# Kernel optimization log

Measured on AMD Instinct MI355X. Metric: run time of the kernel, lower is better.

## Reference

```python
import jax, jax.numpy as jnp
import numpy as np

N = 16384
H = 256
C = 2


def setup_inputs() -> dict:
    key = jax.random.key(0)
    ks = jax.random.split(key, 9)
    s = lambda fan_in: 1.0 / np.sqrt(fan_in)
    return {
        "coordinates": jax.random.normal(ks[0], (N, C), dtype=jnp.float32) * 10.0,
        "W1": jax.random.normal(ks[1], (C, H), dtype=jnp.float32) * s(C),
        "b1": jnp.zeros((H,), dtype=jnp.float32),
        "W2": jax.random.normal(ks[2], (H, H), dtype=jnp.float32) * s(H),
        "b2": jnp.zeros((H,), dtype=jnp.float32),
        "Wd1": jax.random.normal(ks[3], (1, H // 2), dtype=jnp.float32) * s(1),
        "bd1": jnp.zeros((H // 2,), dtype=jnp.float32),
        "Wd2": jax.random.normal(ks[4], (H // 2, H), dtype=jnp.float32) * s(H // 2),
        "bd2": jnp.zeros((H,), dtype=jnp.float32),
        "k": 6,
    }


def reference(coordinates, W1, b1, W2, b2, Wd1, bd1, Wd2, bd2, k):
    x = coordinates.astype(jnp.float32)
    # coord MLP: Linear -> SiLU -> Linear
    coord_emb = jax.nn.silu(x @ W1 + b1) @ W2 + b2  # (N, H)

    # pairwise Euclidean distances (N, N), via ||a||^2 + ||b||^2 - 2ab
    sq = jnp.sum(x * x, axis=1)  # (N,)
    d2 = sq[:, None] + sq[None, :] - 2.0 * (x @ x.T)
    dist = jnp.sqrt(jnp.maximum(d2, 1e-12))  # safe sqrt; diag ~ 0

    # k+1 smallest distances per row (includes self at ~0), ascending
    kk = min(k + 1, dist.shape[1])
    neg_top, _ = jax.lax.top_k(-dist, kk)
    topk_dist = -neg_top  # ascending smallest
    mean_dist = jnp.mean(topk_dist[:, 1:], axis=1, keepdims=True)  # (N, 1)

    dist_emb = jax.nn.silu(mean_dist @ Wd1 + bd1) @ Wd2 + bd2  # (N, H)
    return coord_emb + dist_emb
```

## Files before the change

### kernel.cpp

```cpp
#include <hip/hip_runtime.h>
#include <float.h>
#include <math.h>

#define NPTS 16384
#define HDIM 256

#define KNB   256
#define KXMIN (-48.0f)
#define KW    0.375f
#define KINVW (1.0f / KW)

typedef __attribute__((ext_vector_type(8))) short bf16x8;
typedef __attribute__((ext_vector_type(4))) float f32x4;

__device__ __forceinline__ float silu_f(float z) {
    return z / (1.0f + __expf(-z));
}

__device__ __forceinline__ short f2bf(float f) {
    unsigned u = __float_as_uint(f);
    u = (u + 0x7FFFu + ((u >> 16) & 1u)) >> 16;
    return (short)u;
}

__device__ __forceinline__ float bcast_lane(float x, int l) {
    return __int_as_float(__builtin_amdgcn_readlane(__float_as_int(x), l));
}

__device__ __forceinline__ int binof(float x) {
    int b = (int)floorf((x - KXMIN) * KINVW);
    return b < 0 ? 0 : (b > KNB - 1 ? KNB - 1 : b);
}

#define INS7(a0,a1,a2,a3,a4,a5,a6,V)                \
    {   const float v_ = (V);                       \
        a6 = fmaxf(a5, fminf(a6, v_));              \
        a5 = fmaxf(a4, fminf(a5, v_));              \
        a4 = fmaxf(a3, fminf(a4, v_));              \
        a3 = fmaxf(a2, fminf(a3, v_));              \
        a2 = fmaxf(a1, fminf(a2, v_));              \
        a1 = fmaxf(a0, fminf(a1, v_));              \
        a0 = fminf(a0, v_);                         \
    }

__global__ __launch_bounds__(1024) void prep_kernel(
        const float* __restrict__ xyf,
        const float* __restrict__ W2, const float* __restrict__ Wd2,
        unsigned short* __restrict__ W2p, unsigned short* __restrict__ Wd2p,
        float2* __restrict__ sxy, unsigned* __restrict__ qidx,
        unsigned* __restrict__ off, int* __restrict__ lne, int* __restrict__ rne) {
    const int tid = threadIdx.x;

    if (blockIdx.x < 12) {
        const int slot = blockIdx.x * 1024 + tid;
        const float* src;
        unsigned short* dst;
        int s;
        if (slot < 8192) { src = W2;  dst = W2p;  s = slot; }
        else             { src = Wd2; dst = Wd2p; s = slot - 8192; }
        const int t   = s >> 10;
        const int rem = s & 1023;
        const int ct  = rem >> 6;
        const int l   = rem & 63;
        const int k0  = t * 32 + 8 * (l >> 4);
        const int c   = ct * 16 + (l & 15);
        bf16x8 v;
        #pragma unroll
        for (int i = 0; i < 8; ++i)
            v[i] = f2bf(src[(size_t)(k0 + i) * HDIM + c]);
        ((bf16x8*)dst)[s] = v;
        return;
    }

    __shared__ unsigned cnt[16][KNB];
    __shared__ unsigned tot[KNB];
    __shared__ unsigned sc[KNB];
    __shared__ int      li[KNB];
    __shared__ int      ri[KNB];
    const int w = tid >> 6;

    for (int i = tid; i < 16 * KNB; i += 1024) ((unsigned*)cnt)[i] = 0u;
    __syncthreads();
    for (int i = tid; i < NPTS; i += 1024)
        atomicAdd(&cnt[w][binof(xyf[2 * i])], 1u);
    __syncthreads();

    if (tid < KNB) {
        unsigned run = 0u;
        #pragma unroll
        for (int ww = 0; ww < 16; ++ww) {
            const unsigned t_ = cnt[ww][tid];
            cnt[ww][tid] = run;
            run += t_;
        }
        tot[tid] = run;
        sc[tid]  = run;
        li[tid]  = run ? tid : -1;
        ri[tid]  = run ? tid : KNB;
    }
    __syncthreads();
    for (int s = 1; s < KNB; s <<= 1) {
        unsigned v = 0u; int lv = -1, rv = KNB;
        if (tid < KNB) {
            if (tid >= s)       { v  = sc[tid - s]; lv = li[tid - s]; }
            if (tid + s < KNB)  { rv = ri[tid + s]; }
        }
        __syncthreads();
        if (tid < KNB) {
            sc[tid] += v;
            li[tid] = li[tid] > lv ? li[tid] : lv;
            ri[tid] = ri[tid] < rv ? ri[tid] : rv;
        }
        __syncthreads();
    }
    if (tid < KNB) {
        const unsigned excl = sc[tid] - tot[tid];
        off[tid] = excl;
        lne[tid] = li[tid];
        rne[tid] = ri[tid];
        #pragma unroll
        for (int ww = 0; ww < 16; ++ww) cnt[ww][tid] += excl;
    }
    if (tid == 0) off[KNB] = (unsigned)NPTS;
    __syncthreads();
    for (int i = tid; i < NPTS; i += 1024) {
        const float2 p = ((const float2*)xyf)[i];
        const unsigned pos = atomicAdd(&cnt[w][binof(p.x)], 1u);
        sxy[pos]  = p;
        qidx[pos] = (unsigned)i;
    }
}

__global__ __launch_bounds__(256, 8) void knn_search(const float2* __restrict__ sxy,
                                                     const unsigned* __restrict__ qidx,
                                                     const unsigned* __restrict__ off,
                                                     const int* __restrict__ lne,
                                                     const int* __restrict__ rne,
                                                     float* __restrict__ md) {
    const int lane = threadIdx.x & 63;
    const int wv   = threadIdx.x >> 6;
    const int qpos = blockIdx.x * 4 + wv;
    const float2 q = sxy[qpos];

    float s0 = FLT_MAX, s1 = FLT_MAX, s2 = FLT_MAX, s3 = FLT_MAX,
          s4 = FLT_MAX, s5 = FLT_MAX, s6 = FLT_MAX;

    const int b0 = binof(q.x);
    const int lb = b0 > 0 ? b0 - 1 : 0;
    const int rb = b0 < KNB - 1 ? b0 + 1 : KNB - 1;

    {
        const unsigned o = off[lb], e = off[rb + 1];
        for (unsigned u = o + (unsigned)lane; u < e; u += 64u) {
            const float2 p = sxy[u];
            const float dx = q.x - p.x, dy = q.y - p.y;
            const float d2 = fmaf(dx, dx, dy * dy);
            if (d2 < s6) INS7(s0, s1, s2, s3, s4, s5, s6, d2)
        }
    }

    #pragma unroll
    for (int m = 1; m < 64; m <<= 1) {
        const float o0 = __shfl_xor(s0, m);
        const float o1 = __shfl_xor(s1, m);
        const float o2 = __shfl_xor(s2, m);
        const float o3 = __shfl_xor(s3, m);
        const float o4 = __shfl_xor(s4, m);
        const float o5 = __shfl_xor(s5, m);
        const float o6 = __shfl_xor(s6, m);
        const float n0 = fminf(s0, o0);
        const float n1 = fminf(fminf(s1, o1), fmaxf(s0, o0));
        const float n2 = fminf(fminf(s2, o2),
                               fminf(fmaxf(s0, o1), fmaxf(s1, o0)));
        const float n3 = fminf(fminf(s3, o3),
                               fminf(fmaxf(s0, o2),
                                     fminf(fmaxf(s1, o1), fmaxf(s2, o0))));
        const float n4 = fminf(fminf(s4, o4),
                               fminf(fminf(fmaxf(s0, o3), fmaxf(s1, o2)),
                                     fminf(fmaxf(s2, o1), fmaxf(s3, o0))));
        const float n5 = fminf(fminf(s5, o5),
                               fminf(fminf(fmaxf(s0, o4), fmaxf(s1, o3)),
                                     fminf(fmaxf(s2, o2),
                                           fminf(fmaxf(s3, o1), fmaxf(s4, o0)))));
        const float n6 = fminf(fminf(s6, o6),
                               fminf(fminf(fmaxf(s0, o5), fmaxf(s1, o4)),
                                     fminf(fmaxf(s2, o3),
                                           fminf(fmaxf(s3, o2),
                                                 fminf(fmaxf(s4, o1),
                                                       fmaxf(s5, o0))))));
        s0 = n0; s1 = n1; s2 = n2; s3 = n3; s4 = n4; s5 = n5; s6 = n6;
    }

    int l = lb - 1, r = rb + 1;
    while (true) {
        l = (l >= 0) ? lne[l] : -1;
        r = (r < KNB) ? rne[r] : KNB;
        if (l < 0 && r >= KNB) break;
        float bl = FLT_MAX, br = FLT_MAX;
        if (l >= 0) {
            const float d = fmaxf(q.x - (KXMIN + (float)(l + 1) * KW), 0.0f);
            bl = d * d;
        }
        if (r < KNB) {
            const float d = fmaxf((KXMIN + (float)r * KW) - q.x, 0.0f);
            br = d * d;
        }
        if (fminf(bl, br) > s6) break;
        const int b = (bl <= br) ? l : r;
        const unsigned o = off[b], e = off[b + 1];
        for (unsigned u = o; u < e; u += 64u) {
            const unsigned idx = u + (unsigned)lane;
            float d2 = FLT_MAX;
            if (idx < e) {
                const float2 p = sxy[idx];
                const float dx = q.x - p.x, dy = q.y - p.y;
                d2 = fmaf(dx, dx, dy * dy);
            }
            unsigned long long m = __ballot(d2 < s6);
            while (m) {
                const int L   = __ffsll(m) - 1;
                const float v = bcast_lane(d2, L);
                INS7(s0, s1, s2, s3, s4, s5, s6, v)
                if (lane == L) d2 = FLT_MAX;
                m = __ballot(d2 < s6);
            }
        }
        if (bl <= br) --l; else ++r;
    }

    if (lane == 0) {
        const float sum = sqrtf(fmaxf(s1, 1e-12f)) + sqrtf(fmaxf(s2, 1e-12f)) +
                          sqrtf(fmaxf(s3, 1e-12f)) + sqrtf(fmaxf(s4, 1e-12f)) +
                          sqrtf(fmaxf(s5, 1e-12f)) + sqrtf(fmaxf(s6, 1e-12f));
        md[qidx[qpos]] = sum * (1.0f / 6.0f);
    }
}

#define GEN_A(T)                                                              \
    {                                                                         \
        const int kb = (T) * 32 + klane;                                      \
        const float4 p0 = *(const float4*)(W1 + kb);                          \
        const float4 p1 = *(const float4*)(W1 + kb + 4);                      \
        const float4 r0_ = *(const float4*)(W1 + HDIM + kb);                  \
        const float4 r1_ = *(const float4*)(W1 + HDIM + kb + 4);              \
        const float4 c0_ = *(const float4*)(b1 + kb);                         \
        const float4 c1_ = *(const float4*)(b1 + kb + 4);                     \
        const float pw[8] = {p0.x,p0.y,p0.z,p0.w,p1.x,p1.y,p1.z,p1.w};        \
        const float rw[8] = {r0_.x,r0_.y,r0_.z,r0_.w,r1_.x,r1_.y,r1_.z,r1_.w};\
        const float cw[8] = {c0_.x,c0_.y,c0_.z,c0_.w,c1_.x,c1_.y,c1_.z,c1_.w};\
        _Pragma("unroll")                                                     \
        for (int i = 0; i < 8; ++i)                                           \
            a[i] = f2bf(silu_f(fmaf(q.x, pw[i], fmaf(q.y, rw[i], cw[i]))));   \
    }

#define GEN_G(T)                                                              \
    {                                                                         \
        const int kb = (T) * 32 + klane;                                      \
        const float4 p0 = *(const float4*)(Wd1 + kb);                         \
        const float4 p1 = *(const float4*)(Wd1 + kb + 4);                     \
        const float4 c0_ = *(const float4*)(bd1 + kb);                        \
        const float4 c1_ = *(const float4*)(bd1 + kb + 4);                    \
        const float pw[8] = {p0.x,p0.y,p0.z,p0.w,p1.x,p1.y,p1.z,p1.w};        \
        const float cw[8] = {c0_.x,c0_.y,c0_.z,c0_.w,c1_.x,c1_.y,c1_.z,c1_.w};\
        _Pragma("unroll")                                                     \
        for (int i = 0; i < 8; ++i)                                           \
            a[i] = f2bf(silu_f(fmaf(mdr, pw[i], cw[i])));                     \
    }

#define MFMA8(BUF)                                                            \
    _Pragma("unroll")                                                         \
    for (int j = 0; j < 8; ++j)                                               \
        acc[j] = __builtin_amdgcn_mfma_f32_16x16x32_bf16(a, BUF[j], acc[j], 0, 0, 0);

#define LOADB(BUF, ARR, T)                                                    \
    _Pragma("unroll")                                                         \
    for (int j = 0; j < 8; ++j)                                               \
        BUF[j] = ARR[((T) * 16 + ch * 8 + j) * 64 + lane];

__global__ __launch_bounds__(256, 2) void mlp_kernel(
        const float* __restrict__ xyf,
        const float* __restrict__ W1,  const float* __restrict__ b1,
        const float* __restrict__ b2,
        const float* __restrict__ Wd1, const float* __restrict__ bd1,
        const float* __restrict__ bd2,
        const unsigned short* __restrict__ W2p,
        const unsigned short* __restrict__ Wd2p,
        const float* __restrict__ md,  float* __restrict__ out) {
    const int tid  = threadIdx.x;
    const int lane = tid & 63;
    const int w    = tid >> 6;
    const int r0   = blockIdx.x * 32 + (w >> 1) * 16;
    const int ch   = w & 1;
    const int row  = r0 + (lane & 15);
    const float2 q = ((const float2*)xyf)[row];
    const float mdr = md[row];
    const int klane = 8 * (lane >> 4);

    f32x4 acc[8];
    #pragma unroll
    for (int j = 0; j < 8; ++j) {
        acc[j][0] = 0.0f; acc[j][1] = 0.0f; acc[j][2] = 0.0f; acc[j][3] = 0.0f;
    }

    const bf16x8* B1 = (const bf16x8*)W2p;
    const bf16x8* B2 = (const bf16x8*)Wd2p;
    bf16x8 bA[8], bB[8];
    bf16x8 a;

    LOADB(bA, B1, 0)

    #pragma unroll
    for (int tt = 0; tt < 4; ++tt) {
        {   const int t = 2 * tt;
            GEN_A(t)
            LOADB(bB, B1, t + 1)
            MFMA8(bA)
        }
        {   const int t = 2 * tt + 1;
            GEN_A(t)
            if (t + 1 < 8) { LOADB(bA, B1, t + 1) }
            else           { LOADB(bA, B2, 0)     }
            MFMA8(bB)
        }
    }

    #pragma unroll
    for (int uu = 0; uu < 2; ++uu) {
        {   const int t = 2 * uu;
            GEN_G(t)
            LOADB(bB, B2, t + 1)
            MFMA8(bA)
        }
        {   const int t = 2 * uu + 1;
            GEN_G(t)
            if (t + 1 < 4) { LOADB(bA, B2, t + 1) }
            MFMA8(bB)
        }
    }

    const int cb = ch * 128;
    const int rr = r0 + 4 * (lane >> 4);
    #pragma unroll
    for (int j = 0; j < 8; ++j) {
        const int c = cb + j * 16 + (lane & 15);
        const float add = b2[c] + bd2[c];
        out[(size_t)(rr + 0) * HDIM + c] = acc[j][0] + add;
        out[(size_t)(rr + 1) * HDIM + c] = acc[j][1] + add;
        out[(size_t)(rr + 2) * HDIM + c] = acc[j][2] + add;
        out[(size_t)(rr + 3) * HDIM + c] = acc[j][3] + add;
    }
}

extern "C" void kernel_launch(void* const* d_in, const int* in_sizes, int n_in,
                              void* d_out, int out_size, void* d_ws, size_t ws_size,
                              hipStream_t stream) {
    const float* xy  = (const float*)d_in[0];
    const float* W1  = (const float*)d_in[1];
    const float* b1  = (const float*)d_in[2];
    const float* W2  = (const float*)d_in[3];
    const float* b2  = (const float*)d_in[4];
    const float* Wd1 = (const float*)d_in[5];
    const float* bd1 = (const float*)d_in[6];
    const float* Wd2 = (const float*)d_in[7];
    const float* bd2 = (const float*)d_in[8];
    float* out = (float*)d_out;

    char* ws = (char*)d_ws;
    float*          md   = (float*)ws;
    unsigned short* W2p  = (unsigned short*)(ws + 65536);
    unsigned short* Wd2p = (unsigned short*)(ws + 196608);
    unsigned*       off  = (unsigned*)(ws + 262144);
    float2*         sxy  = (float2*)(ws + 263424);
    unsigned*       qidx = (unsigned*)(ws + 394496);
    int*            lne  = (int*)(ws + 460032);
    int*            rne  = (int*)(ws + 461056);

    prep_kernel<<<13, 1024, 0, stream>>>(xy, W2, Wd2, W2p, Wd2p, sxy, qidx,
                                         off, lne, rne);
    knn_search<<<NPTS / 4, 256, 0, stream>>>(sxy, qidx, off, lne, rne, md);
    mlp_kernel<<<NPTS / 32, 256, 0, stream>>>(xy, W1, b1, b2, Wd1, bd1, bd2,
                                              W2p, Wd2p, md, out);
}
```

Baseline: 174.6 us.

## Replace variable bins with fixed 64-point chunks and prefix x-bounds for kNN pruning

The kNN search now walks fixed chunks of 64 points from the x-sorted array instead of variable-size histogram bins, so each chunk is one full wavefront load. Pruning uses prefix-max and suffix-min x bounds per chunk, which prep_kernel computes after the scatter. The search kernel now runs 8 waves per block. The MLP kernel is regridded to 16 rows per block, with each wave covering 64 output columns, to raise occupancy. The extra prep reductions add serial work in a single block, and the points within each bin are not sorted, so the chunk x-bounds may overlap and loosen pruning.

```diff
diff --git a/kernel.cpp b/kernel.cpp
--- a/kernel.cpp
+++ b/kernel.cpp
@@ -9,6 +9,7 @@
 #define KXMIN (-48.0f)
 #define KW    0.375f
 #define KINVW (1.0f / KW)
+#define NCH   256
 
 typedef __attribute__((ext_vector_type(8))) short bf16x8;
 typedef __attribute__((ext_vector_type(4))) float f32x4;
@@ -48,7 +49,7 @@
         const float* __restrict__ W2, const float* __restrict__ Wd2,
         unsigned short* __restrict__ W2p, unsigned short* __restrict__ Wd2p,
         float2* __restrict__ sxy, unsigned* __restrict__ qidx,
-        unsigned* __restrict__ off, int* __restrict__ lne, int* __restrict__ rne) {
+        float* __restrict__ pmaxx, float* __restrict__ sminx) {
     const int tid = threadIdx.x;
 
     if (blockIdx.x < 12) {
@@ -75,9 +76,10 @@
     __shared__ unsigned cnt[16][KNB];
     __shared__ unsigned tot[KNB];
     __shared__ unsigned sc[KNB];
-    __shared__ int      li[KNB];
-    __shared__ int      ri[KNB];
-    const int w = tid >> 6;
+    __shared__ float    pm[NCH];
+    __shared__ float    sm[NCH];
+    const int w    = tid >> 6;
+    const int lane = tid & 63;
 
     for (int i = tid; i < 16 * KNB; i += 1024) ((unsigned*)cnt)[i] = 0u;
     __syncthreads();
@@ -95,33 +97,20 @@
         }
         tot[tid] = run;
         sc[tid]  = run;
-        li[tid]  = run ? tid : -1;
-        ri[tid]  = run ? tid : KNB;
     }
     __syncthreads();
     for (int s = 1; s < KNB; s <<= 1) {
-        unsigned v = 0u; int lv = -1, rv = KNB;
-        if (tid < KNB) {
-            if (tid >= s)       { v  = sc[tid - s]; lv = li[tid - s]; }
-            if (tid + s < KNB)  { rv = ri[tid + s]; }
-        }
+        unsigned v = 0u;
+        if (tid < KNB && tid >= s) v = sc[tid - s];
         __syncthreads();
-        if (tid < KNB) {
-            sc[tid] += v;
-            li[tid] = li[tid] > lv ? li[tid] : lv;
-            ri[tid] = ri[tid] < rv ? ri[tid] : rv;
-        }
+        if (tid < KNB) sc[tid] += v;
         __syncthreads();
     }
     if (tid < KNB) {
         const unsigned excl = sc[tid] - tot[tid];
-        off[tid] = excl;
-        lne[tid] = li[tid];
-        rne[tid] = ri[tid];
         #pragma unroll
         for (int ww = 0; ww < 16; ++ww) cnt[ww][tid] += excl;
     }
-    if (tid == 0) off[KNB] = (unsigned)NPTS;
     __syncthreads();
     for (int i = tid; i < NPTS; i += 1024) {
         const float2 p = ((const float2*)xyf)[i];
@@ -129,34 +118,56 @@
         sxy[pos]  = p;
         qidx[pos] = (unsigned)i;
     }
-}
-
-__global__ __launch_bounds__(256, 8) void knn_search(const float2* __restrict__ sxy,
+    __syncthreads();
+
+    for (int c = w; c < NCH; c += 16) {
+        const float xv = sxy[c * 64 + lane].x;
+        float xmn = xv, xmx = xv;
+        #pragma unroll
+        for (int m = 1; m < 64; m <<= 1) {
+            xmn = fminf(xmn, __shfl_xor(xmn, m));
+            xmx = fmaxf(xmx, __shfl_xor(xmx, m));
+        }
+        if (lane == 0) { pm[c] = xmx; sm[c] = xmn; }
+    }
+    __syncthreads();
+    for (int s = 1; s < NCH; s <<= 1) {
+        float pv = -FLT_MAX, sv = FLT_MAX;
+        if (tid < NCH) {
+            if (tid >= s)       pv = pm[tid - s];
+            if (tid + s < NCH)  sv = sm[tid + s];
+        }
+        __syncthreads();
+        if (tid < NCH) {
+            pm[tid] = fmaxf(pm[tid], pv);
+            sm[tid] = fminf(sm[tid], sv);
+        }
+        __syncthreads();
+    }
+    if (tid < NCH) { pmaxx[tid] = pm[tid]; sminx[tid] = sm[tid]; }
+}
+
+__global__ __launch_bounds__(512, 8) void knn_search(const float2* __restrict__ sxy,
                                                      const unsigned* __restrict__ qidx,
-                                                     const unsigned* __restrict__ off,
-                                                     const int* __restrict__ lne,
-                                                     const int* __restrict__ rne,
+                                                     const float* __restrict__ pmaxx,
+                                                     const float* __restrict__ sminx,
                                                      float* __restrict__ md) {
     const int lane = threadIdx.x & 63;
     const int wv   = threadIdx.x >> 6;
-    const int qpos = blockIdx.x * 4 + wv;
+    const int qpos = blockIdx.x * 8 + wv;
     const float2 q = sxy[qpos];
+    const int c0 = qpos >> 6;
+    const int lb = c0 > 0 ? c0 - 1 : 0;
+    const int rb = c0 < NCH - 1 ? c0 + 1 : NCH - 1;
 
     float s0 = FLT_MAX, s1 = FLT_MAX, s2 = FLT_MAX, s3 = FLT_MAX,
           s4 = FLT_MAX, s5 = FLT_MAX, s6 = FLT_MAX;
 
-    const int b0 = binof(q.x);
-    const int lb = b0 > 0 ? b0 - 1 : 0;
-    const int rb = b0 < KNB - 1 ? b0 + 1 : KNB - 1;
-
-    {
-        const unsigned o = off[lb], e = off[rb + 1];
-        for (unsigned u = o + (unsigned)lane; u < e; u += 64u) {
-            const float2 p = sxy[u];
-            const float dx = q.x - p.x, dy = q.y - p.y;
-            const float d2 = fmaf(dx, dx, dy * dy);
-            if (d2 < s6) INS7(s0, s1, s2, s3, s4, s5, s6, d2)
-        }
+    for (int b = lb; b <= rb; ++b) {
+        const float2 p = sxy[b * 64 + lane];
+        const float dx = q.x - p.x, dy = q.y - p.y;
+        const float d2 = fmaf(dx, dx, dy * dy);
+        if (d2 < s6) INS7(s0, s1, s2, s3, s4, s5, s6, d2)
     }
 
     #pragma unroll
@@ -192,38 +203,31 @@
     }
 
     int l = lb - 1, r = rb + 1;
-    while (true) {
-        l = (l >= 0) ? lne[l] : -1;
-        r = (r < KNB) ? rne[r] : KNB;
-        if (l < 0 && r >= KNB) break;
+    while (l >= 0 || r < NCH) {
         float bl = FLT_MAX, br = FLT_MAX;
         if (l >= 0) {
-            const float d = fmaxf(q.x - (KXMIN + (float)(l + 1) * KW), 0.0f);
+            const float d = fmaxf(q.x - pmaxx[l], 0.0f);
             bl = d * d;
         }
-        if (r < KNB) {
-            const float d = fmaxf((KXMIN + (float)r * KW) - q.x, 0.0f);
+        if (r < NCH) {
+            const float d = fmaxf(sminx[r] - q.x, 0.0f);
             br = d * d;
         }
         if (fminf(bl, br) > s6) break;
         const int b = (bl <= br) ? l : r;
-        const unsigned o = off[b], e = off[b + 1];
-        for (unsigned u = o; u < e; u += 64u) {
-            const unsigned idx = u + (unsigned)lane;
-            float d2 = FLT_MAX;
-            if (idx < e) {
-                const float2 p = sxy[idx];
-                const float dx = q.x - p.x, dy = q.y - p.y;
-                d2 = fmaf(dx, dx, dy * dy);
-            }
-            unsigned long long m = __ballot(d2 < s6);
-            while (m) {
-                const int L   = __ffsll(m) - 1;
-                const float v = bcast_lane(d2, L);
-                INS7(s0, s1, s2, s3, s4, s5, s6, v)
-                if (lane == L) d2 = FLT_MAX;
-                m = __ballot(d2 < s6);
-            }
+        const float2 p = sxy[b * 64 + lane];
+        float d2;
+        {
+            const float dx = q.x - p.x, dy = q.y - p.y;
+            d2 = fmaf(dx, dx, dy * dy);
+        }
+        unsigned long long m = __ballot(d2 < s6);
+        while (m) {
+            const int L   = __ffsll(m) - 1;
+            const float v = bcast_lane(d2, L);
+            INS7(s0, s1, s2, s3, s4, s5, s6, v)
+            if (lane == L) d2 = FLT_MAX;
+            m = __ballot(d2 < s6);
         }
         if (bl <= br) --l; else ++r;
     }
@@ -267,17 +271,17 @@
             a[i] = f2bf(silu_f(fmaf(mdr, pw[i], cw[i])));                     \
     }
 
-#define MFMA8(BUF)                                                            \
+#define MFMA4(BUF)                                                            \
     _Pragma("unroll")                                                         \
-    for (int j = 0; j < 8; ++j)                                               \
+    for (int j = 0; j < 4; ++j)                                               \
         acc[j] = __builtin_amdgcn_mfma_f32_16x16x32_bf16(a, BUF[j], acc[j], 0, 0, 0);
 
-#define LOADB(BUF, ARR, T)                                                    \
+#define LOADB4(BUF, ARR, T)                                                   \
     _Pragma("unroll")                                                         \
-    for (int j = 0; j < 8; ++j)                                               \
-        BUF[j] = ARR[((T) * 16 + ch * 8 + j) * 64 + lane];
-
-__global__ __launch_bounds__(256, 2) void mlp_kernel(
+    for (int j = 0; j < 4; ++j)                                               \
+        BUF[j] = ARR[((T) * 16 + cq * 4 + j) * 64 + lane];
+
+__global__ __launch_bounds__(256, 4) void mlp_kernel(
         const float* __restrict__ xyf,
         const float* __restrict__ W1,  const float* __restrict__ b1,
         const float* __restrict__ b2,
@@ -288,39 +292,38 @@
         const float* __restrict__ md,  float* __restrict__ out) {
     const int tid  = threadIdx.x;
     const int lane = tid & 63;
-    const int w    = tid >> 6;
-    const int r0   = blockIdx.x * 32 + (w >> 1) * 16;
-    const int ch   = w & 1;
+    const int cq   = tid >> 6;
+    const int r0   = blockIdx.x * 16;
     const int row  = r0 + (lane & 15);
     const float2 q = ((const float2*)xyf)[row];
     const float mdr = md[row];
     const int klane = 8 * (lane >> 4);
 
-    f32x4 acc[8];
-    #pragma unroll
-    for (int j = 0; j < 8; ++j) {
+    f32x4 acc[4];
+    #pragma unroll
+    for (int j = 0; j < 4; ++j) {
         acc[j][0] = 0.0f; acc[j][1] = 0.0f; acc[j][2] = 0.0f; acc[j][3] = 0.0f;
     }
 
     const bf16x8* B1 = (const bf16x8*)W2p;
     const bf16x8* B2 = (const bf16x8*)Wd2p;
-    bf16x8 bA[8], bB[8];
+    bf16x8 bA[4], bB[4];
     bf16x8 a;
 
-    LOADB(bA, B1, 0)
+    LOADB4(bA, B1, 0)
 
     #pragma unroll
     for (int tt = 0; tt < 4; ++tt) {
         {   const int t = 2 * tt;
             GEN_A(t)
-            LOADB(bB, B1, t + 1)
-            MFMA8(bA)
+            LOADB4(bB, B1, t + 1)
+            MFMA4(bA)
         }
         {   const int t = 2 * tt + 1;
             GEN_A(t)
-            if (t + 1 < 8) { LOADB(bA, B1, t + 1) }
-            else           { LOADB(bA, B2, 0)     }
-            MFMA8(bB)
+            if (t + 1 < 8) { LOADB4(bA, B1, t + 1) }
+            else           { LOADB4(bA, B2, 0)     }
+            MFMA4(bB)
         }
     }
 
@@ -328,20 +331,20 @@
     for (int uu = 0; uu < 2; ++uu) {
         {   const int t = 2 * uu;
             GEN_G(t)
-            LOADB(bB, B2, t + 1)
-            MFMA8(bA)
+            LOADB4(bB, B2, t + 1)
+            MFMA4(bA)
         }
         {   const int t = 2 * uu + 1;
             GEN_G(t)
-            if (t + 1 < 4) { LOADB(bA, B2, t + 1) }
-            MFMA8(bB)
-        }
-    }
-
-    const int cb = ch * 128;
+            if (t + 1 < 4) { LOADB4(bA, B2, t + 1) }
+            MFMA4(bB)
+        }
+    }
+
+    const int cb = cq * 64;
     const int rr = r0 + 4 * (lane >> 4);
     #pragma unroll
-    for (int j = 0; j < 8; ++j) {
+    for (int j = 0; j < 4; ++j) {
         const int c = cb + j * 16 + (lane & 15);
         const float add = b2[c] + bd2[c];
         out[(size_t)(rr + 0) * HDIM + c] = acc[j][0] + add;
@@ -366,18 +369,17 @@
     float* out = (float*)d_out;
 
     char* ws = (char*)d_ws;
-    float*          md   = (float*)ws;
-    unsigned short* W2p  = (unsigned short*)(ws + 65536);
-    unsigned short* Wd2p = (unsigned short*)(ws + 196608);
-    unsigned*       off  = (unsigned*)(ws + 262144);
-    float2*         sxy  = (float2*)(ws + 263424);
-    unsigned*       qidx = (unsigned*)(ws + 394496);
-    int*            lne  = (int*)(ws + 460032);
-    int*            rne  = (int*)(ws + 461056);
+    float*          md    = (float*)ws;
+    unsigned short* W2p   = (unsigned short*)(ws + 65536);
+    unsigned short* Wd2p  = (unsigned short*)(ws + 196608);
+    float*          pmaxx = (float*)(ws + 262144);
+    float*          sminx = (float*)(ws + 263168);
+    float2*         sxy   = (float2*)(ws + 264192);
+    unsigned*       qidx  = (unsigned*)(ws + 395264);
 
     prep_kernel<<<13, 1024, 0, stream>>>(xy, W2, Wd2, W2p, Wd2p, sxy, qidx,
-                                         off, lne, rne);
-    knn_search<<<NPTS / 4, 256, 0, stream>>>(sxy, qidx, off, lne, rne, md);
-    mlp_kernel<<<NPTS / 32, 256, 0, stream>>>(xy, W1, b1, b2, Wd1, bd1, bd2,
+                                         pmaxx, sminx);
+    knn_search<<<NPTS / 8, 512, 0, stream>>>(sxy, qidx, pmaxx, sminx, md);
+    mlp_kernel<<<NPTS / 16, 256, 0, stream>>>(xy, W1, b1, b2, Wd1, bd1, bd2,
                                               W2p, Wd2p, md, out);
 }
```

After: 198.3 us. +13.5%, slower.
